# Performance work log

Measured on AMD Instinct MI355X. Metric: run time of the kernel, lower is better.

Reference implementation:

```python
import jax, jax.numpy as jnp
import numpy as np

D_MODEL = 1024
N_HEADS = 16
HDIM = D_MODEL // N_HEADS
IMP_EPS = 1e-6


def setup_inputs() -> dict:
    key = jax.random.key(0)
    ks = jax.random.split(key, 7)
    B, T_q, T_kv, N_s = 2, 2048, 256, 16
    scale = 1.0 / np.sqrt(D_MODEL)
    return {
        "query": jax.random.normal(ks[0], (B, T_q, D_MODEL), dtype=jnp.float32),
        "key_value": jax.random.normal(ks[1], (B, T_kv, N_s, D_MODEL), dtype=jnp.float32),
        "imp_weights": jax.random.uniform(ks[2], (B, N_s), dtype=jnp.float32),
        "W_q": jax.random.normal(ks[3], (D_MODEL, D_MODEL), dtype=jnp.float32) * scale,
        "W_k": jax.random.normal(ks[4], (D_MODEL, D_MODEL), dtype=jnp.float32) * scale,
        "W_v": jax.random.normal(ks[5], (D_MODEL, D_MODEL), dtype=jnp.float32) * scale,
        "W_o": jax.random.normal(ks[6], (D_MODEL, D_MODEL), dtype=jnp.float32) * scale,
    }


def _split_heads(x):
    # [B, T, D] -> [B, h, T, d]
    B, T, _ = x.shape
    return x.reshape(B, T, N_HEADS, HDIM).transpose(0, 2, 1, 3)


def reference(query, key_value, imp_weights, W_q, W_k, W_v, W_o):
    # CAU_MultiheadCrossAttention.forward with 4D key_value (sensor axis).
    B, T_q, D = query.shape
    _, T_kv, N_s, _ = key_value.shape
    kv = key_value.reshape(B, T_kv * N_s, D)  # flatten sensor axis into source length S

    qh = _split_heads(query @ W_q.T)   # [B,h,T_q,d]  (nn.Linear: x @ W.T)
    kh = _split_heads(kv @ W_k.T)      # [B,h,S,d]
    vh = _split_heads(kv @ W_v.T)      # [B,h,S,d]

    # importance: [B,N_s] -> tiled over T_kv -> [B, S], log-clamped additive mask
    imp_full = jnp.broadcast_to(imp_weights[:, None, :], (B, T_kv, N_s)).reshape(B, T_kv * N_s)
    log_imp = jnp.log(jnp.clip(imp_full, IMP_EPS, None)).astype(qh.dtype)  # [B,S]

    scores = jnp.einsum("bhqd,bhkd->bhqk", qh, kh) / np.sqrt(HDIM).astype(np.float32)
    scores = scores + log_imp[:, None, None, :]
    attn = jax.nn.softmax(scores, axis=-1)
    y = jnp.einsum("bhqk,bhkd->bhqd", attn, vh)  # [B,h,T_q,d]

    y = y.transpose(0, 2, 1, 3).reshape(B, T_q, D)  # merge heads
    return y @ W_o.T
```

## Files before the change

### kernel.cpp

```cpp
#include <hip/hip_runtime.h>
#include <hip/hip_bf16.h>

typedef __bf16    bf16x8_t __attribute__((ext_vector_type(8)));
typedef __bf16    bf16x4_t __attribute__((ext_vector_type(4)));
typedef float     f32x4_t  __attribute__((ext_vector_type(4)));
typedef _Float16  f16x8_t  __attribute__((ext_vector_type(8)));

static __device__ __forceinline__ f32x4_t mfma16(bf16x8_t a, bf16x8_t b, f32x4_t c) {
    return __builtin_amdgcn_mfma_f32_16x16x32_bf16(a, b, c, 0, 0, 0);
}

static __device__ __forceinline__ float redsum16(float v) {
#pragma unroll
    for (int off = 1; off < 16; off <<= 1) v += __shfl_xor(v, off);
    return v;
}

static __device__ __forceinline__ void async16(const __bf16* g, __bf16* l) {
    __builtin_amdgcn_global_load_lds(
        (const __attribute__((address_space(1))) unsigned int*)g,
        (__attribute__((address_space(3))) unsigned int*)l, 16, 0, 0);
}

__global__ __launch_bounds__(256) void f2b_multi(const float* __restrict__ q,
                                                 const float* __restrict__ kv,
                                                 const float* __restrict__ wq,
                                                 const float* __restrict__ wk,
                                                 const float* __restrict__ wv,
                                                 const float* __restrict__ wo,
                                                 __bf16* __restrict__ qb,
                                                 __bf16* __restrict__ kvb,
                                                 __bf16* __restrict__ wqb,
                                                 __bf16* __restrict__ wkvb,
                                                 __bf16* __restrict__ wob,
                                                 float qscale) {
    int i = blockIdx.x * 256 + threadIdx.x;
    const float* src; __bf16* dst; int base; float scale = 1.0f;
    if (i < 1048576)      { src = q;  dst = qb;   base = 0; }
    else if (i < 3145728) { src = kv; dst = kvb;  base = 1048576; }
    else if (i < 3407872) { src = wq; dst = wqb;  base = 3145728; scale = qscale; }
    else if (i < 3670016) { src = wk; dst = wkvb; base = 3407872; }
    else if (i < 3932160) { src = wv; dst = wkvb + 1048576; base = 3670016; }
    else                  { src = wo; dst = wob;  base = 3932160; }
    int j = i - base;
    float4 v = reinterpret_cast<const float4*>(src)[j];
    bf16x4_t o;
    o[0] = (__bf16)(v.x * scale); o[1] = (__bf16)(v.y * scale);
    o[2] = (__bf16)(v.z * scale); o[3] = (__bf16)(v.w * scale);
    reinterpret_cast<bf16x4_t*>(dst)[j] = o;
}

template <int OMAP, typename CT>
__global__ __launch_bounds__(256) void gemm_bt_kernel(const __bf16* __restrict__ A,
                                                      const __bf16* __restrict__ B,
                                                      CT* __restrict__ C,
                                                      int M, int N, int K,
                                                      __bf16* __restrict__ V2,
                                                      const float* __restrict__ imp) {
    __shared__ __bf16 As[128 * 32];
    __shared__ __bf16 Bs[128 * 32];
    __shared__ __bf16 Es[2][4096];

    const int t    = threadIdx.x;
    const int w    = t >> 6;
    const int lane = t & 63;
    const int quad = lane >> 4;
    const int mn   = lane & 15;
    const int wm   = (w & 1) * 64;
    const int wn   = (w >> 1) * 64;
    const long m0  = (long)blockIdx.y * 128;
    const long n0  = (long)blockIdx.x * 128;

    const int  srow = t >> 2;
    const int  scol = (t & 3) * 8;
    const __bf16* gA = A + (m0 + srow) * (long)K + scol;
    const __bf16* gB = B + (n0 + srow) * (long)K + scol;

    f32x4_t acc[4][4];
#pragma unroll
    for (int i = 0; i < 4; i++)
#pragma unroll
        for (int j = 0; j < 4; j++) acc[i][j] = (f32x4_t){0.f, 0.f, 0.f, 0.f};

    for (int k0 = 0; k0 < K; k0 += 32) {
        __syncthreads();
        async16(gA + k0,                &As[t * 8]);
        async16(gA + (long)64 * K + k0, &As[2048 + t * 8]);
        async16(gB + k0,                &Bs[t * 8]);
        async16(gB + (long)64 * K + k0, &Bs[2048 + t * 8]);
        __syncthreads();

        bf16x8_t af[4], bf[4];
#pragma unroll
        for (int i = 0; i < 4; i++)
            af[i] = *(const bf16x8_t*)&As[(wm + i * 16 + mn) * 32 + quad * 8];
#pragma unroll
        for (int j = 0; j < 4; j++)
            bf[j] = *(const bf16x8_t*)&Bs[(wn + j * 16 + mn) * 32 + quad * 8];
#pragma unroll
        for (int i = 0; i < 4; i++)
#pragma unroll
            for (int j = 0; j < 4; j++) acc[i][j] = mfma16(af[i], bf[j], acc[i][j]);
    }

    if (OMAP == 0) {
#pragma unroll
        for (int i = 0; i < 4; i++)
#pragma unroll
            for (int j = 0; j < 4; j++)
#pragma unroll
                for (int r = 0; r < 4; r++) {
                    long row = m0 + wm + i * 16 + quad * 4 + r;
                    long col = n0 + wn + j * 16 + mn;
                    C[row * N + col] = (CT)acc[i][j][r];
                }
    } else {
        __syncthreads();
        __bf16* stg = (w == 0) ? As : (w == 1) ? Bs : Es[w - 2];
        const bool vpart = (OMAP == 1) && (blockIdx.x >= 8);

        if (OMAP == 2 || !vpart) {
#pragma unroll
            for (int i = 0; i < 4; i++)
#pragma unroll
                for (int j = 0; j < 4; j++)
#pragma unroll
                    for (int r = 0; r < 4; r++) {
                        int sl = i * 16 + quad * 4 + r;
                        int d  = j * 16 + mn;
                        stg[sl * 64 + (((d >> 3) ^ (sl & 7)) * 8) + (d & 7)] =
                            (__bf16)acc[i][j][r];
                    }
        } else {
            const int b_ = (int)((m0 + wm) >> 12);
#pragma unroll
            for (int r = 0; r < 4; r++) {
                float scl = fmaxf(imp[b_ * 16 + quad * 4 + r], 1e-6f);
#pragma unroll
                for (int j = 0; j < 4; j++) {
                    bf16x4_t pk;
#pragma unroll
                    for (int i = 0; i < 4; i++) pk[i] = (__bf16)(acc[i][j][r] * scl);
                    int d  = j * 16 + mn;
                    int p0 = (quad * 4 + r) * 4;
                    *(bf16x4_t*)&stg[d * 64 + (((p0 >> 3) ^ (d & 7)) * 8) + (p0 & 7)] = pk;
                }
            }
        }

        if (OMAP == 2) {
            __bf16* Cg = (__bf16*)C + (m0 + wm) * (long)N + (n0 + wn);
#pragma unroll
            for (int it = 0; it < 8; it++) {
                int rowL = it * 8 + (lane >> 3);
                int cb   = lane & 7;
                bf16x8_t vv = *(const bf16x8_t*)&stg[rowL * 64 + ((cb ^ (rowL & 7)) * 8)];
                *(bf16x8_t*)&Cg[(long)rowL * N + cb * 8] = vv;
            }
        } else {
            const int b_    = (int)((m0 + wm) >> 12);
            const int sbase = (int)((m0 + wm) & 4095);
            __bf16* dst;
            if (!vpart) {
                int h_ = (int)((n0 + wn) >> 6);
                dst = (__bf16*)C + (long)(b_ * 16 + h_) * 262144 + (long)sbase * 64;
            } else {
                int h_ = (int)((n0 + wn) >> 6) - 16;
                dst = V2 + (long)(b_ * 16 + h_) * 262144 + (long)(sbase >> 6) * 4096;
            }
#pragma unroll
            for (int it = 0; it < 8; it++) {
                int rowL = it * 8 + (lane >> 3);
                int cb   = lane & 7;
                bf16x8_t vv = *(const bf16x8_t*)&stg[rowL * 64 + ((cb ^ (rowL & 7)) * 8)];
                *(bf16x8_t*)&dst[rowL * 64 + cb * 8] = vv;
            }
        }
    }
}

__global__ __launch_bounds__(256, 4) void attn_kernel(const __bf16* __restrict__ Qp,
                                                      const __bf16* __restrict__ Kh,
                                                      const __bf16* __restrict__ Vh,
                                                      const float* __restrict__ imp,
                                                      _Float16* __restrict__ Op,
                                                      float* __restrict__ Lp) {
    const int gid = blockIdx.x;
    const int qt  = (gid >> 3) & 15;
    const int sp  = (gid >> 7) & 1;
    const int bh  = ((gid >> 8) << 3) | (gid & 7);
    const int b   = bh >> 4;
    const int h   = bh & 15;
    const int t    = threadIdx.x;
    const int w    = t >> 6;
    const int lane = t & 63;
    const int quad = lane >> 4;
    const int mn   = lane & 15;

    __shared__ __bf16 Ks[64 * 64];
    __shared__ __bf16 Vs[64 * 64];
    __shared__ __bf16 Ps[4][32][72];

    const long qrow0 = (long)b * 2048 + qt * 128 + w * 32;
    const __bf16* Kb = Kh + (long)bh * 262144;
    const __bf16* Vb = Vh + (long)bh * 262144;

    const int r8 = lane >> 3;
    const int cs = (lane & 7) ^ r8;
    const int srcoff0 = (0 * 4 + w) * 512 + r8 * 64 + cs * 8;
    const int srcoff1 = (1 * 4 + w) * 512 + r8 * 64 + cs * 8;
    __bf16* ldsK0 = Ks + (0 * 4 + w) * 512;
    __bf16* ldsK1 = Ks + (1 * 4 + w) * 512;
    __bf16* ldsV0 = Vs + (0 * 4 + w) * 512;
    __bf16* ldsV1 = Vs + (1 * 4 + w) * 512;

    bf16x8_t aq[2][2];
#pragma unroll
    for (int rt = 0; rt < 2; rt++)
#pragma unroll
        for (int x = 0; x < 2; x++)
            aq[rt][x] = *(const bf16x8_t*)&Qp[(qrow0 + rt * 16 + mn) * 1024 + h * 64 + x * 32 + quad * 8];

    const float impc = fmaxf(imp[b * 16 + mn], 1e-6f);

    float lpart[2][4];
    f32x4_t o[2][4];
#pragma unroll
    for (int rt = 0; rt < 2; rt++)
#pragma unroll
        for (int r = 0; r < 4; r++) lpart[rt][r] = 0.f;
#pragma unroll
    for (int rt = 0; rt < 2; rt++)
#pragma unroll
        for (int dt = 0; dt < 4; dt++) o[rt][dt] = (f32x4_t){0.f, 0.f, 0.f, 0.f};

    for (int st = sp * 32; st < sp * 32 + 32; st++) {
        const long kbase = (long)st * 4096;
        __syncthreads();
        async16(Kb + kbase + srcoff0, ldsK0);
        async16(Kb + kbase + srcoff1, ldsK1);
        async16(Vb + kbase + srcoff0, ldsV0);
        async16(Vb + kbase + srcoff1, ldsV1);
        __syncthreads();

        f32x4_t sc[2][4];
        {
            bf16x8_t bk0[4], bk1[4];
#pragma unroll
            for (int ct = 0; ct < 4; ct++) {
                int s  = ct * 16 + mn;
                int c0 = (quad ^ (s & 7)) * 8;
                bk0[ct] = *(const bf16x8_t*)&Ks[s * 64 + c0];
                bk1[ct] = *(const bf16x8_t*)&Ks[s * 64 + (c0 ^ 32)];
            }
#pragma unroll
            for (int rt = 0; rt < 2; rt++) {
#pragma unroll
                for (int ct = 0; ct < 4; ct++) sc[rt][ct] = (f32x4_t){0.f, 0.f, 0.f, 0.f};
#pragma unroll
                for (int ct = 0; ct < 4; ct++) {
                    sc[rt][ct] = mfma16(aq[rt][0], bk0[ct], sc[rt][ct]);
                    sc[rt][ct] = mfma16(aq[rt][1], bk1[ct], sc[rt][ct]);
                }
            }
        }

#pragma unroll
        for (int rt = 0; rt < 2; rt++)
#pragma unroll
            for (int r = 0; r < 4; r++) {
                float p0 = __builtin_amdgcn_exp2f(sc[rt][0][r]);
                float p1 = __builtin_amdgcn_exp2f(sc[rt][1][r]);
                float p2 = __builtin_amdgcn_exp2f(sc[rt][2][r]);
                float p3 = __builtin_amdgcn_exp2f(sc[rt][3][r]);
                lpart[rt][r] += (p0 + p1) + (p2 + p3);
                bf16x4_t pk;
                pk[0] = (__bf16)p0; pk[1] = (__bf16)p1;
                pk[2] = (__bf16)p2; pk[3] = (__bf16)p3;
                *(bf16x4_t*)&Ps[w][rt * 16 + quad * 4 + r][mn * 4] = pk;
            }

        {
            bf16x8_t bv0[4], bv1[4];
#pragma unroll
            for (int dt = 0; dt < 4; dt++) {
                int d  = dt * 16 + mn;
                int c0 = (quad ^ (d & 7)) * 8;
                bv0[dt] = *(const bf16x8_t*)&Vs[d * 64 + c0];
                bv1[dt] = *(const bf16x8_t*)&Vs[d * 64 + (c0 ^ 32)];
            }
#pragma unroll
            for (int rt = 0; rt < 2; rt++) {
                bf16x8_t ap0 = *(const bf16x8_t*)&Ps[w][rt * 16 + mn][quad * 8];
                bf16x8_t ap1 = *(const bf16x8_t*)&Ps[w][rt * 16 + mn][32 + quad * 8];
#pragma unroll
                for (int dt = 0; dt < 4; dt++) {
                    o[rt][dt] = mfma16(ap0, bv0[dt], o[rt][dt]);
                    o[rt][dt] = mfma16(ap1, bv1[dt], o[rt][dt]);
                }
            }
        }
    }

#pragma unroll
    for (int rt = 0; rt < 2; rt++)
#pragma unroll
        for (int r = 0; r < 4; r++) {
            float l = redsum16(lpart[rt][r] * impc);
            long row = qrow0 + rt * 16 + quad * 4 + r;
            if (mn == 0) Lp[((long)sp * 4096 + row) * 16 + h] = l;
#pragma unroll
            for (int dt = 0; dt < 4; dt++)
                Op[((long)sp * 4096 + row) * 1024 + h * 64 + dt * 16 + mn] =
                    (_Float16)o[rt][dt][r];
        }
}

__global__ __launch_bounds__(256) void combine_kernel(const _Float16* __restrict__ Op,
                                                      const float* __restrict__ Lp,
                                                      __bf16* __restrict__ Y) {
    int tid = blockIdx.x * 256 + threadIdx.x;
    int row = tid >> 7;
    int cg  = tid & 127;
    int h   = cg >> 3;
    f16x8_t o0 = *(const f16x8_t*)&Op[(long)row * 1024 + cg * 8];
    f16x8_t o1 = *(const f16x8_t*)&Op[(long)(4096 + row) * 1024 + cg * 8];
    float inv = 1.0f / (Lp[row * 16 + h] + Lp[(4096 + row) * 16 + h]);
    bf16x8_t y;
#pragma unroll
    for (int j = 0; j < 8; j++) y[j] = (__bf16)(((float)o0[j] + (float)o1[j]) * inv);
    *(bf16x8_t*)&Y[(long)row * 1024 + cg * 8] = y;
}

extern "C" void kernel_launch(void* const* d_in, const int* in_sizes, int n_in,
                              void* d_out, int out_size, void* d_ws, size_t ws_size,
                              hipStream_t stream) {
    const float* q_f  = (const float*)d_in[0];
    const float* kv_f = (const float*)d_in[1];
    const float* imp  = (const float*)d_in[2];
    const float* wq_f = (const float*)d_in[3];
    const float* wk_f = (const float*)d_in[4];
    const float* wv_f = (const float*)d_in[5];
    const float* wo_f = (const float*)d_in[6];

    char* ws = (char*)d_ws;
    const size_t MB = 1ull << 20;
    __bf16*   qb    = (__bf16*)(ws + 0);
    __bf16*   kvb   = (__bf16*)(ws + 8 * MB);
    __bf16*   wqb   = (__bf16*)(ws + 24 * MB);
    __bf16*   wkvb  = (__bf16*)(ws + 26 * MB);
    _Float16* Opart = (_Float16*)(ws + 0);
    float*    Lpart = (float*)(ws + 16 * MB);
    __bf16*   Yb    = (__bf16*)(ws + 17 * MB);
    __bf16*   wob   = (__bf16*)(ws + 30 * MB);
    __bf16*   Qp    = (__bf16*)(ws + 32 * MB);
    __bf16*   Khd   = (__bf16*)(ws + 40 * MB);
    __bf16*   Vhd   = (__bf16*)(ws + 56 * MB);

    const float QSCALE = 0.125f * 1.4426950408889634f;

    f2b_multi<<<16384, 256, 0, stream>>>(q_f, kv_f, wq_f, wk_f, wv_f, wo_f,
                                         qb, kvb, wqb, wkvb, wob, QSCALE);

    gemm_bt_kernel<2, __bf16><<<dim3(8, 32), 256, 0, stream>>>(qb, wqb, Qp, 4096, 1024, 1024,
                                                               nullptr, nullptr);
    gemm_bt_kernel<1, __bf16><<<dim3(16, 64), 256, 0, stream>>>(kvb, wkvb, Khd, 8192, 2048, 1024,
                                                                Vhd, imp);

    attn_kernel<<<1024, 256, 0, stream>>>(Qp, Khd, Vhd, imp, Opart, Lpart);
    combine_kernel<<<2048, 256, 0, stream>>>(Opart, Lpart, Yb);

    gemm_bt_kernel<0, float><<<dim3(8, 32), 256, 0, stream>>>(Yb, wob, (float*)d_out, 4096, 1024, 1024,
                                                              nullptr, nullptr);
}
```

Baseline: 299.2 us.

## Merge Q and KV projections into one launch and double-buffer attention K/V tiles

The separate Q projection and K/V projection GEMM launches become a single 1280-block kernel that picks its mode from the block index. This removes one launch and the tail idle time between the two GEMMs. The attention kernel now double-buffers its K/V LDS tiles, prefetching the next tile during compute and needing one barrier per iteration instead of two. It also drops the launch-bounds occupancy hint of 4 blocks per CU, and its LDS use doubles, which may lower occupancy.

```diff
diff --git a/kernel.cpp b/kernel.cpp
--- a/kernel.cpp
+++ b/kernel.cpp
@@ -50,16 +50,30 @@
     reinterpret_cast<bf16x4_t*>(dst)[j] = o;
 }
 
-template <int OMAP, typename CT>
-__global__ __launch_bounds__(256) void gemm_bt_kernel(const __bf16* __restrict__ A,
-                                                      const __bf16* __restrict__ B,
-                                                      CT* __restrict__ C,
-                                                      int M, int N, int K,
-                                                      __bf16* __restrict__ V2,
-                                                      const float* __restrict__ imp) {
+__global__ __launch_bounds__(256) void proj_kernel(const __bf16* __restrict__ qb,
+                                                   const __bf16* __restrict__ wqb,
+                                                   const __bf16* __restrict__ kvb,
+                                                   const __bf16* __restrict__ wkvb,
+                                                   __bf16* __restrict__ Qp,
+                                                   __bf16* __restrict__ Khd,
+                                                   __bf16* __restrict__ Vhd,
+                                                   const float* __restrict__ imp) {
     __shared__ __bf16 As[128 * 32];
     __shared__ __bf16 Bs[128 * 32];
     __shared__ __bf16 Es[2][4096];
+
+    const int gid = blockIdx.x;
+    const __bf16 *A, *B;
+    long m0, n0;
+    int mode;
+    if (gid < 256) {
+        m0 = (long)(gid >> 3) * 128; n0 = (long)(gid & 7) * 128;
+        A = qb; B = wqb; mode = 0;
+    } else {
+        int g2 = gid - 256;
+        m0 = (long)(g2 >> 4) * 128; n0 = (long)(g2 & 15) * 128;
+        A = kvb; B = wkvb; mode = (n0 < 1024) ? 1 : 2;
+    }
 
     const int t    = threadIdx.x;
     const int w    = t >> 6;
@@ -68,13 +82,11 @@
     const int mn   = lane & 15;
     const int wm   = (w & 1) * 64;
     const int wn   = (w >> 1) * 64;
-    const long m0  = (long)blockIdx.y * 128;
-    const long n0  = (long)blockIdx.x * 128;
 
     const int  srow = t >> 2;
     const int  scol = (t & 3) * 8;
-    const __bf16* gA = A + (m0 + srow) * (long)K + scol;
-    const __bf16* gB = B + (n0 + srow) * (long)K + scol;
+    const __bf16* gA = A + (m0 + srow) * 1024 + scol;
+    const __bf16* gB = B + (n0 + srow) * 1024 + scol;
 
     f32x4_t acc[4][4];
 #pragma unroll
@@ -82,12 +94,12 @@
 #pragma unroll
         for (int j = 0; j < 4; j++) acc[i][j] = (f32x4_t){0.f, 0.f, 0.f, 0.f};
 
-    for (int k0 = 0; k0 < K; k0 += 32) {
+    for (int k0 = 0; k0 < 1024; k0 += 32) {
         __syncthreads();
-        async16(gA + k0,                &As[t * 8]);
-        async16(gA + (long)64 * K + k0, &As[2048 + t * 8]);
-        async16(gB + k0,                &Bs[t * 8]);
-        async16(gB + (long)64 * K + k0, &Bs[2048 + t * 8]);
+        async16(gA + k0,              &As[t * 8]);
+        async16(gA + 64 * 1024 + k0,  &As[2048 + t * 8]);
+        async16(gB + k0,              &Bs[t * 8]);
+        async16(gB + 64 * 1024 + k0,  &Bs[2048 + t * 8]);
         __syncthreads();
 
         bf16x8_t af[4], bf[4];
@@ -103,88 +115,74 @@
             for (int j = 0; j < 4; j++) acc[i][j] = mfma16(af[i], bf[j], acc[i][j]);
     }
 
-    if (OMAP == 0) {
+    __syncthreads();
+    __bf16* stg = (w == 0) ? As : (w == 1) ? Bs : Es[w - 2];
+
+    if (mode != 2) {
 #pragma unroll
         for (int i = 0; i < 4; i++)
 #pragma unroll
             for (int j = 0; j < 4; j++)
 #pragma unroll
                 for (int r = 0; r < 4; r++) {
-                    long row = m0 + wm + i * 16 + quad * 4 + r;
-                    long col = n0 + wn + j * 16 + mn;
-                    C[row * N + col] = (CT)acc[i][j][r];
+                    int sl = i * 16 + quad * 4 + r;
+                    int d  = j * 16 + mn;
+                    stg[sl * 64 + (((d >> 3) ^ (sl & 7)) * 8) + (d & 7)] =
+                        (__bf16)acc[i][j][r];
                 }
     } else {
-        __syncthreads();
-        __bf16* stg = (w == 0) ? As : (w == 1) ? Bs : Es[w - 2];
-        const bool vpart = (OMAP == 1) && (blockIdx.x >= 8);
-
-        if (OMAP == 2 || !vpart) {
-#pragma unroll
-            for (int i = 0; i < 4; i++)
-#pragma unroll
-                for (int j = 0; j < 4; j++)
-#pragma unroll
-                    for (int r = 0; r < 4; r++) {
-                        int sl = i * 16 + quad * 4 + r;
-                        int d  = j * 16 + mn;
-                        stg[sl * 64 + (((d >> 3) ^ (sl & 7)) * 8) + (d & 7)] =
-                            (__bf16)acc[i][j][r];
-                    }
+        const int b_ = (int)((m0 + wm) >> 12);
+#pragma unroll
+        for (int r = 0; r < 4; r++) {
+            float scl = fmaxf(imp[b_ * 16 + quad * 4 + r], 1e-6f);
+#pragma unroll
+            for (int j = 0; j < 4; j++) {
+                bf16x4_t pk;
+#pragma unroll
+                for (int i = 0; i < 4; i++) pk[i] = (__bf16)(acc[i][j][r] * scl);
+                int d  = j * 16 + mn;
+                int p0 = (quad * 4 + r) * 4;
+                *(bf16x4_t*)&stg[d * 64 + (((p0 >> 3) ^ (d & 7)) * 8) + (p0 & 7)] = pk;
+            }
+        }
+    }
+
+    if (mode == 0) {
+        __bf16* Cg = Qp + (m0 + wm) * 1024 + (n0 + wn);
+#pragma unroll
+        for (int it = 0; it < 8; it++) {
+            int rowL = it * 8 + (lane >> 3);
+            int cb   = lane & 7;
+            bf16x8_t vv = *(const bf16x8_t*)&stg[rowL * 64 + ((cb ^ (rowL & 7)) * 8)];
+            *(bf16x8_t*)&Cg[(long)rowL * 1024 + cb * 8] = vv;
+        }
+    } else {
+        const int b_    = (int)((m0 + wm) >> 12);
+        const int sbase = (int)((m0 + wm) & 4095);
+        __bf16* dst;
+        if (mode == 1) {
+            int h_ = (int)((n0 + wn) >> 6);
+            dst = Khd + (long)(b_ * 16 + h_) * 262144 + (long)sbase * 64;
         } else {
-            const int b_ = (int)((m0 + wm) >> 12);
-#pragma unroll
-            for (int r = 0; r < 4; r++) {
-                float scl = fmaxf(imp[b_ * 16 + quad * 4 + r], 1e-6f);
-#pragma unroll
-                for (int j = 0; j < 4; j++) {
-                    bf16x4_t pk;
-#pragma unroll
-                    for (int i = 0; i < 4; i++) pk[i] = (__bf16)(acc[i][j][r] * scl);
-                    int d  = j * 16 + mn;
-                    int p0 = (quad * 4 + r) * 4;
-                    *(bf16x4_t*)&stg[d * 64 + (((p0 >> 3) ^ (d & 7)) * 8) + (p0 & 7)] = pk;
-                }
-            }
-        }
-
-        if (OMAP == 2) {
-            __bf16* Cg = (__bf16*)C + (m0 + wm) * (long)N + (n0 + wn);
-#pragma unroll
-            for (int it = 0; it < 8; it++) {
-                int rowL = it * 8 + (lane >> 3);
-                int cb   = lane & 7;
-                bf16x8_t vv = *(const bf16x8_t*)&stg[rowL * 64 + ((cb ^ (rowL & 7)) * 8)];
-                *(bf16x8_t*)&Cg[(long)rowL * N + cb * 8] = vv;
-            }
-        } else {
-            const int b_    = (int)((m0 + wm) >> 12);
-            const int sbase = (int)((m0 + wm) & 4095);
-            __bf16* dst;
-            if (!vpart) {
-                int h_ = (int)((n0 + wn) >> 6);
-                dst = (__bf16*)C + (long)(b_ * 16 + h_) * 262144 + (long)sbase * 64;
-            } else {
-                int h_ = (int)((n0 + wn) >> 6) - 16;
-                dst = V2 + (long)(b_ * 16 + h_) * 262144 + (long)(sbase >> 6) * 4096;
-            }
-#pragma unroll
-            for (int it = 0; it < 8; it++) {
-                int rowL = it * 8 + (lane >> 3);
-                int cb   = lane & 7;
-                bf16x8_t vv = *(const bf16x8_t*)&stg[rowL * 64 + ((cb ^ (rowL & 7)) * 8)];
-                *(bf16x8_t*)&dst[rowL * 64 + cb * 8] = vv;
-            }
-        }
-    }
-}
-
-__global__ __launch_bounds__(256, 4) void attn_kernel(const __bf16* __restrict__ Qp,
-                                                      const __bf16* __restrict__ Kh,
-                                                      const __bf16* __restrict__ Vh,
-                                                      const float* __restrict__ imp,
-                                                      _Float16* __restrict__ Op,
-                                                      float* __restrict__ Lp) {
+            int h_ = (int)((n0 + wn) >> 6) - 16;
+            dst = Vhd + (long)(b_ * 16 + h_) * 262144 + (long)(sbase >> 6) * 4096;
+        }
+#pragma unroll
+        for (int it = 0; it < 8; it++) {
+            int rowL = it * 8 + (lane >> 3);
+            int cb   = lane & 7;
+            bf16x8_t vv = *(const bf16x8_t*)&stg[rowL * 64 + ((cb ^ (rowL & 7)) * 8)];
+            *(bf16x8_t*)&dst[rowL * 64 + cb * 8] = vv;
+        }
+    }
+}
+
+__global__ __launch_bounds__(256) void attn_kernel(const __bf16* __restrict__ Qp,
+                                                   const __bf16* __restrict__ Kh,
+                                                   const __bf16* __restrict__ Vh,
+                                                   const float* __restrict__ imp,
+                                                   _Float16* __restrict__ Op,
+                                                   float* __restrict__ Lp) {
     const int gid = blockIdx.x;
     const int qt  = (gid >> 3) & 15;
     const int sp  = (gid >> 7) & 1;
@@ -197,8 +195,8 @@
     const int quad = lane >> 4;
     const int mn   = lane & 15;
 
-    __shared__ __bf16 Ks[64 * 64];
-    __shared__ __bf16 Vs[64 * 64];
+    __shared__ __bf16 Ks[2][4096];
+    __shared__ __bf16 Vs[2][4096];
     __shared__ __bf16 Ps[4][32][72];
 
     const long qrow0 = (long)b * 2048 + qt * 128 + w * 32;
@@ -209,10 +207,6 @@
     const int cs = (lane & 7) ^ r8;
     const int srcoff0 = (0 * 4 + w) * 512 + r8 * 64 + cs * 8;
     const int srcoff1 = (1 * 4 + w) * 512 + r8 * 64 + cs * 8;
-    __bf16* ldsK0 = Ks + (0 * 4 + w) * 512;
-    __bf16* ldsK1 = Ks + (1 * 4 + w) * 512;
-    __bf16* ldsV0 = Vs + (0 * 4 + w) * 512;
-    __bf16* ldsV1 = Vs + (1 * 4 + w) * 512;
 
     bf16x8_t aq[2][2];
 #pragma unroll
@@ -234,14 +228,25 @@
 #pragma unroll
         for (int dt = 0; dt < 4; dt++) o[rt][dt] = (f32x4_t){0.f, 0.f, 0.f, 0.f};
 
-    for (int st = sp * 32; st < sp * 32 + 32; st++) {
-        const long kbase = (long)st * 4096;
+    {
+        const long kbase = (long)(sp * 32) * 4096;
+        async16(Kb + kbase + srcoff0, &Ks[0][(0 * 4 + w) * 512]);
+        async16(Kb + kbase + srcoff1, &Ks[0][(1 * 4 + w) * 512]);
+        async16(Vb + kbase + srcoff0, &Vs[0][(0 * 4 + w) * 512]);
+        async16(Vb + kbase + srcoff1, &Vs[0][(1 * 4 + w) * 512]);
+    }
+
+    for (int ii = 0; ii < 32; ii++) {
+        const int bi = ii & 1;
         __syncthreads();
-        async16(Kb + kbase + srcoff0, ldsK0);
-        async16(Kb + kbase + srcoff1, ldsK1);
-        async16(Vb + kbase + srcoff0, ldsV0);
-        async16(Vb + kbase + srcoff1, ldsV1);
-        __syncthreads();
+
+        if (ii + 1 < 32) {
+            const long kbase = (long)(sp * 32 + ii + 1) * 4096;
+            async16(Kb + kbase + srcoff0, &Ks[bi ^ 1][(0 * 4 + w) * 512]);
+            async16(Kb + kbase + srcoff1, &Ks[bi ^ 1][(1 * 4 + w) * 512]);
+            async16(Vb + kbase + srcoff0, &Vs[bi ^ 1][(0 * 4 + w) * 512]);
+            async16(Vb + kbase + srcoff1, &Vs[bi ^ 1][(1 * 4 + w) * 512]);
+        }
 
         f32x4_t sc[2][4];
         {
@@ -250,8 +255,8 @@
             for (int ct = 0; ct < 4; ct++) {
                 int s  = ct * 16 + mn;
                 int c0 = (quad ^ (s & 7)) * 8;
-                bk0[ct] = *(const bf16x8_t*)&Ks[s * 64 + c0];
-                bk1[ct] = *(const bf16x8_t*)&Ks[s * 64 + (c0 ^ 32)];
+                bk0[ct] = *(const bf16x8_t*)&Ks[bi][s * 64 + c0];
+                bk1[ct] = *(const bf16x8_t*)&Ks[bi][s * 64 + (c0 ^ 32)];
             }
 #pragma unroll
             for (int rt = 0; rt < 2; rt++) {
@@ -286,8 +291,8 @@
             for (int dt = 0; dt < 4; dt++) {
                 int d  = dt * 16 + mn;
                 int c0 = (quad ^ (d & 7)) * 8;
-                bv0[dt] = *(const bf16x8_t*)&Vs[d * 64 + c0];
-                bv1[dt] = *(const bf16x8_t*)&Vs[d * 64 + (c0 ^ 32)];
+                bv0[dt] = *(const bf16x8_t*)&Vs[bi][d * 64 + c0];
+                bv1[dt] = *(const bf16x8_t*)&Vs[bi][d * 64 + (c0 ^ 32)];
             }
 #pragma unroll
             for (int rt = 0; rt < 2; rt++) {
@@ -330,6 +335,66 @@
 #pragma unroll
     for (int j = 0; j < 8; j++) y[j] = (__bf16)(((float)o0[j] + (float)o1[j]) * inv);
     *(bf16x8_t*)&Y[(long)row * 1024 + cg * 8] = y;
+}
+
+__global__ __launch_bounds__(256) void gemm_out_kernel(const __bf16* __restrict__ A,
+                                                       const __bf16* __restrict__ B,
+                                                       float* __restrict__ C) {
+    __shared__ __bf16 As[128 * 32];
+    __shared__ __bf16 Bs[128 * 32];
+
+    const int t    = threadIdx.x;
+    const int w    = t >> 6;
+    const int lane = t & 63;
+    const int quad = lane >> 4;
+    const int mn   = lane & 15;
+    const int wm   = (w & 1) * 64;
+    const int wn   = (w >> 1) * 64;
+    const long m0  = (long)blockIdx.y * 128;
+    const long n0  = (long)blockIdx.x * 128;
+
+    const int  srow = t >> 2;
+    const int  scol = (t & 3) * 8;
+    const __bf16* gA = A + (m0 + srow) * 1024 + scol;
+    const __bf16* gB = B + (n0 + srow) * 1024 + scol;
+
+    f32x4_t acc[4][4];
+#pragma unroll
+    for (int i = 0; i < 4; i++)
+#pragma unroll
+        for (int j = 0; j < 4; j++) acc[i][j] = (f32x4_t){0.f, 0.f, 0.f, 0.f};
+
+    for (int k0 = 0; k0 < 1024; k0 += 32) {
+        __syncthreads();
+        async16(gA + k0,             &As[t * 8]);
+        async16(gA + 64 * 1024 + k0, &As[2048 + t * 8]);
+        async16(gB + k0,             &Bs[t * 8]);
+        async16(gB + 64 * 1024 + k0, &Bs[2048 + t * 8]);
+        __syncthreads();
+
+        bf16x8_t af[4], bf[4];
+#pragma unroll
+        for (int i = 0; i < 4; i++)
+            af[i] = *(const bf16x8_t*)&As[(wm + i * 16 + mn) * 32 + quad * 8];
+#pragma unroll
+        for (int j = 0; j < 4; j++)
+            bf[j] = *(const bf16x8_t*)&Bs[(wn + j * 16 + mn) * 32 + quad * 8];
+#pragma unroll
+        for (int i = 0; i < 4; i++)
+#pragma unroll
+            for (int j = 0; j < 4; j++) acc[i][j] = mfma16(af[i], bf[j], acc[i][j]);
+    }
+
+#pragma unroll
+    for (int i = 0; i < 4; i++)
+#pragma unroll
+        for (int j = 0; j < 4; j++)
+#pragma unroll
+            for (int r = 0; r < 4; r++) {
+                long row = m0 + wm + i * 16 + quad * 4 + r;
+                long col = n0 + wn + j * 16 + mn;
+                C[row * 1024 + col] = acc[i][j][r];
+            }
 }
 
 extern "C" void kernel_launch(void* const* d_in, const int* in_sizes, int n_in,
@@ -362,14 +427,10 @@
     f2b_multi<<<16384, 256, 0, stream>>>(q_f, kv_f, wq_f, wk_f, wv_f, wo_f,
                                          qb, kvb, wqb, wkvb, wob, QSCALE);
 
-    gemm_bt_kernel<2, __bf16><<<dim3(8, 32), 256, 0, stream>>>(qb, wqb, Qp, 4096, 1024, 1024,
-                                                               nullptr, nullptr);
-    gemm_bt_kernel<1, __bf16><<<dim3(16, 64), 256, 0, stream>>>(kvb, wkvb, Khd, 8192, 2048, 1024,
-                                                                Vhd, imp);
+    proj_kernel<<<1280, 256, 0, stream>>>(qb, wqb, kvb, wkvb, Qp, Khd, Vhd, imp);
 
     attn_kernel<<<1024, 256, 0, stream>>>(Qp, Khd, Vhd, imp, Opart, Lpart);
     combine_kernel<<<2048, 256, 0, stream>>>(Opart, Lpart, Yb);
 
-    gemm_bt_kernel<0, float><<<dim3(8, 32), 256, 0, stream>>>(Yb, wob, (float*)d_out, 4096, 1024, 1024,
-                                                              nullptr, nullptr);
-}
+    gemm_out_kernel<<<dim3(8, 32), 256, 0, stream>>>(Yb, wob, (float*)d_out);
+}
```

New measurement: 304.3 us. About the same (+1.7%).
